# Kernel optimization log

Measured on AMD Instinct MI355X. Metric: run time of the kernel, lower is better.

Reference implementation:

```python
import jax, jax.numpy as jnp
import numpy as np

N0, N1, N2 = 100000, 25000, 6250
E0, E1, E2 = 600000, 150000, 40000
K = 6
NUM_CLASSES = 10


def setup_inputs() -> dict:
    key = jax.random.key(0)
    ks = jax.random.split(key, 20)
    inp = {
        "pos": jax.random.normal(ks[0], (N0, 3), dtype=jnp.float32),
        "edge_index0": jax.random.randint(ks[1], (2, E0), 0, N0, dtype=jnp.int32),
        "edge_index1": jax.random.randint(ks[2], (2, E1), 0, N1, dtype=jnp.int32),
        "edge_index2": jax.random.randint(ks[3], (2, E2), 0, N2, dtype=jnp.int32),
        "d0_rows": jax.random.randint(ks[4], (N0,), 0, N1, dtype=jnp.int32),
        "d0_cols": jax.random.randint(ks[5], (N0,), 0, N0, dtype=jnp.int32),
        "d0_vals": jax.random.uniform(ks[6], (N0,), dtype=jnp.float32),
        "d1_rows": jax.random.randint(ks[7], (N1,), 0, N2, dtype=jnp.int32),
        "d1_cols": jax.random.randint(ks[8], (N1,), 0, N1, dtype=jnp.int32),
        "d1_vals": jax.random.uniform(ks[9], (N1,), dtype=jnp.float32),
        "W0": jax.random.normal(ks[10], (K, 3, 32), dtype=jnp.float32) * 0.1,
        "b0": jax.random.normal(ks[11], (32,), dtype=jnp.float32) * 0.1,
        "W1": jax.random.normal(ks[12], (K, 32, 64), dtype=jnp.float32) * 0.1,
        "b1": jax.random.normal(ks[13], (64,), dtype=jnp.float32) * 0.1,
        "W2": jax.random.normal(ks[14], (K, 64, 128), dtype=jnp.float32) * 0.1,
        "b2": jax.random.normal(ks[15], (128,), dtype=jnp.float32) * 0.1,
        "lin_w": jax.random.normal(ks[16], (NUM_CLASSES, N2 * 128), dtype=jnp.float32) * 0.01,
        "lin_b": jax.random.normal(ks[17], (NUM_CLASSES,), dtype=jnp.float32) * 0.1,
    }
    return inp


def _cheb_edge_weights(row, col, n):
    # PyG get_laplacian(sym) followed by 2L/lambda_max - I with lambda_max=2:
    # diagonal becomes 0, off-diagonal weight = -deg^{-1/2}[row] * deg^{-1/2}[col]
    deg = jax.ops.segment_sum(jnp.ones(row.shape[0], jnp.float32), row, num_segments=n)
    dinv = jnp.where(deg > 0, 1.0 / jnp.sqrt(deg), 0.0)
    return -dinv[row] * dinv[col]


def _cheb_conv(x, edge_index, W, b, n):
    # Chebyshev recurrence: Tx0 = x, Tx1 = L_hat x, Tx_k = 2 L_hat Tx_{k-1} - Tx_{k-2}
    row, col = edge_index[0], edge_index[1]
    w = _cheb_edge_weights(row, col, n)

    def prop(z):  # [n, C] -> [n, C] scatter-gather over edges
        return jax.ops.segment_sum(w[:, None] * z[col], row, num_segments=n)

    Tx0 = x
    out = Tx0 @ W[0]
    Tx1 = prop(x)
    out = out + Tx1 @ W[1]
    for k in range(2, W.shape[0]):
        Tx2 = 2.0 * prop(Tx1) - Tx0
        out = out + Tx2 @ W[k]
        Tx0, Tx1 = Tx1, Tx2
    return out + b


def _pool(x, rows, cols, vals, n_out):
    # torch.sparse.mm(D, x) with D given in COO form
    return jax.ops.segment_sum(vals[:, None] * x[cols], rows, num_segments=n_out)


def reference(pos, edge_index0, edge_index1, edge_index2,
              d0_rows, d0_cols, d0_vals, d1_rows, d1_cols, d1_vals,
              W0, b0, W1, b1, W2, b2, lin_w, lin_b):
    x = jax.nn.relu(_cheb_conv(pos, edge_index0, W0, b0, N0))
    x = _pool(x, d0_rows, d0_cols, d0_vals, N1)
    x = jax.nn.relu(_cheb_conv(x, edge_index1, W1, b1, N1))
    x = _pool(x, d1_rows, d1_cols, d1_vals, N2)
    x = _cheb_conv(x, edge_index2, W2, b2, N2)  # no ReLU on last conv
    Z = lin_w @ x.reshape(-1) + lin_b
    return Z
```

## Files before the change

### kernel.cpp

```cpp
#include <hip/hip_runtime.h>


#define TPB 256
#define NB   318
#define BCAP 8192
#define EPB  4096
#define TXS  800000LL

static inline int gs(long long n) { return (int)((n + TPB - 1) / TPB); }

struct Desc5 {
    const int* rows[5];
    const int* cols[5];
    const float* vals[5];
    int eoff[6];
    int doff[5];
};


__global__ void k_binA_pad(Desc5 d, int* __restrict__ gbcnt, int2* __restrict__ binrec,
                           int Etot, int binBlocks,
                           const float* __restrict__ pos, float4* __restrict__ pdst,
                           int npos) {
    __shared__ int2 srec[EPB];
    __shared__ unsigned short sbuck[EPB];
    __shared__ int scnt[NB], sbase[NB], slcur[NB];
    int tid = threadIdx.x;
    if ((int)blockIdx.x >= binBlocks) {
        int i = (blockIdx.x - binBlocks) * 256 + tid;
        if (i < npos)
            pdst[i] = make_float4(pos[3 * i], pos[3 * i + 1], pos[3 * i + 2], 0.f);
        return;
    }
    int e0 = blockIdx.x * EPB;
    int ne = min(EPB, Etot - e0);
    for (int b = tid; b < NB; b += 256) scnt[b] = 0;
    __syncthreads();
    for (int i = tid; i < ne; i += 256) {
        int e = e0 + i;
        int s = 0;
        while (e >= d.eoff[s + 1]) ++s;
        int le = e - d.eoff[s];
        int grow = d.doff[s] + d.rows[s][le];
        int col = d.cols[s][le];
        int vb = (s >= 3) ? __float_as_int(d.vals[s][le]) : 0;
        int b = grow >> 9;
        srec[i] = make_int2(((grow & 511) << 17) | col, vb);
        sbuck[i] = (unsigned short)b;
        atomicAdd(&scnt[b], 1);
    }
    __syncthreads();
    for (int b = tid; b < NB; b += 256) {
        sbase[b] = scnt[b] > 0 ? atomicAdd(&gbcnt[b], scnt[b]) : 0;
        slcur[b] = 0;
    }
    __syncthreads();
    for (int i = tid; i < ne; i += 256) {
        int b = sbuck[i];
        int off = atomicAdd(&slcur[b], 1);
        binrec[(long long)b * BCAP + sbase[b] + off] = srec[i];
    }
}

__global__ void k_B1(const int* __restrict__ gbcnt, const int2* __restrict__ binrec,
                     int* __restrict__ rowptr, float* __restrict__ dinv,
                     int ntot, int ndinv, int Etot) {
    __shared__ int cnt[512], lexcl[512], wsum[4];
    int bucket = blockIdx.x, tid = threadIdx.x;
    int lane = tid & 63, wid = tid >> 6;
    {
        int v0 = (2 * tid < NB) ? gbcnt[2 * tid] : 0;
        int v1 = (2 * tid + 1 < NB) ? gbcnt[2 * tid + 1] : 0;
        int p = v0 + v1;
        int s = p;
#pragma unroll
        for (int off = 1; off < 64; off <<= 1) {
            int t = __shfl_up(s, off, 64);
            if (lane >= off) s += t;
        }
        if (lane == 63) wsum[wid] = s;
        __syncthreads();
        int add = 0;
        for (int w = 0; w < wid; ++w) add += wsum[w];
        int ep = add + s - p;
        lexcl[2 * tid] = ep; lexcl[2 * tid + 1] = ep + v0;
        __syncthreads();
    }
    int base = lexcl[bucket];
    __syncthreads();
    int ne = gbcnt[bucket];
    const int2* br = binrec + (long long)bucket * BCAP;
    cnt[2 * tid] = 0; cnt[2 * tid + 1] = 0;
    __syncthreads();
    for (int i = tid; i < ne; i += 256)
        atomicAdd(&cnt[br[i].x >> 17], 1);
    __syncthreads();
    int c0 = cnt[2 * tid], c1 = cnt[2 * tid + 1], p = c0 + c1;
    int s = p;
#pragma unroll
    for (int off = 1; off < 64; off <<= 1) {
        int t = __shfl_up(s, off, 64);
        if (lane >= off) s += t;
    }
    if (lane == 63) wsum[wid] = s;
    __syncthreads();
    int add = 0;
    for (int w = 0; w < wid; ++w) add += wsum[w];
    int ep = add + s - p;
    lexcl[2 * tid] = ep; lexcl[2 * tid + 1] = ep + c0;
    __syncthreads();
    int row0 = bucket << 9;
    int nrows = min(512, ntot - row0);
    for (int lr = tid; lr < nrows; lr += 256) {
        int grow = row0 + lr;
        rowptr[grow] = base + lexcl[lr];
        if (grow < ndinv) {
            int c = cnt[lr];
            dinv[grow] = c > 0 ? 1.0f / sqrtf((float)c) : 0.f;
        }
    }
    if (bucket == 0 && tid == 0) rowptr[ntot] = Etot;
}

__global__ void k_B2(const int* __restrict__ gbcnt, const int2* __restrict__ binrec,
                     const int* __restrict__ rowptr, const float* __restrict__ dinv,
                     int2* __restrict__ rec, int ntot) {
    __shared__ int lbase[512], lcur[512];
    int bucket = blockIdx.x, tid = threadIdx.x;
    int row0 = bucket << 9;
    for (int i = tid; i < 512; i += 256) {
        int grow = row0 + i;
        lbase[i] = (grow < ntot) ? rowptr[grow] : 0;
        lcur[i] = 0;
    }
    __syncthreads();
    int ne = gbcnt[bucket];
    const int2* br = binrec + (long long)bucket * BCAP;
    for (int i = tid; i < ne; i += 256) {
        int2 r = br[i];
        int lr = r.x >> 17, col = r.x & 0x1FFFF;
        int grow = row0 + lr;
        int pos = lbase[lr] + atomicAdd(&lcur[lr], 1);
        float wv;
        if (grow < 100000)      wv = dinv[col];
        else if (grow < 125000) wv = dinv[100000 + col];
        else if (grow < 131250) wv = dinv[125000 + col];
        else                    wv = __int_as_float(r.y);
        rec[pos] = make_int2(col, __float_as_int(wv));
    }
}


__global__ void k_sprop_c4p(const int* __restrict__ rowptr, const int2* __restrict__ rec,
                            const float* __restrict__ dinv, const float* __restrict__ src,
                            const float* __restrict__ prev, float* __restrict__ dst,
                            int n, int mode) {
    int idx = blockIdx.x * blockDim.x + threadIdx.x;
    if (idx >= 2 * n) return;
    int r = idx >> 1, half = idx & 1;
    int s0 = rowptr[r], s1 = rowptr[r + 1];
    float4 a0 = make_float4(0.f, 0.f, 0.f, 0.f), a1 = a0;
    int j = s0 + half;
    for (; j + 2 < s1; j += 4) {
        int2 r0 = rec[j], r1 = rec[j + 2];
        float w0 = __int_as_float(r0.y), w1 = __int_as_float(r1.y);
        float4 s0v = *(const float4*)(src + (long long)r0.x * 4);
        float4 s1v = *(const float4*)(src + (long long)r1.x * 4);
        a0.x += w0 * s0v.x; a0.y += w0 * s0v.y; a0.z += w0 * s0v.z; a0.w += w0 * s0v.w;
        a1.x += w1 * s1v.x; a1.y += w1 * s1v.y; a1.z += w1 * s1v.z; a1.w += w1 * s1v.w;
    }
    if (j < s1) {
        int2 rr = rec[j];
        float w = __int_as_float(rr.y);
        float4 s = *(const float4*)(src + (long long)rr.x * 4);
        a0.x += w * s.x; a0.y += w * s.y; a0.z += w * s.z; a0.w += w * s.w;
    }
    a0.x += a1.x; a0.y += a1.y; a0.z += a1.z; a0.w += a1.w;
    a0.x += __shfl_xor(a0.x, 1, 64);
    a0.y += __shfl_xor(a0.y, 1, 64);
    a0.z += __shfl_xor(a0.z, 1, 64);
    a0.w += __shfl_xor(a0.w, 1, 64);
    if (half == 0) {
        float m = -dinv[r];
        long long o = (long long)r * 4;
        float4 out;
        if (mode) {
            float4 p = *(const float4*)(prev + o);
            out.x = 2.f * m * a0.x - p.x; out.y = 2.f * m * a0.y - p.y;
            out.z = 2.f * m * a0.z - p.z; out.w = 2.f * m * a0.w - p.w;
        } else {
            out.x = m * a0.x; out.y = m * a0.y; out.z = m * a0.z; out.w = m * a0.w;
        }
        *(float4*)(dst + o) = out;
    }
}

__device__ __forceinline__
void sprop32p_body(const int* __restrict__ rowptr, const int2* __restrict__ rec,
                   const float* __restrict__ dinv, const float* __restrict__ src,
                   const float* __restrict__ prev, float* __restrict__ dst,
                   int n, int mode, int idx) {
    constexpr int C = 32;
    if (idx >= n * 8) return;
    int cid = idx >> 1, half = idx & 1;
    int r = cid >> 2, c4 = (cid & 3) * 8;
    int s0 = rowptr[r], s1 = rowptr[r + 1];
    float4 a0 = make_float4(0.f, 0.f, 0.f, 0.f), a1 = a0;
    for (int j = s0 + half; j < s1; j += 2) {
        int2 rr = rec[j];
        float w = __int_as_float(rr.y);
        const float* sp = src + (long long)rr.x * C + c4;
        float4 s0v = *(const float4*)(sp);
        float4 s1v = *(const float4*)(sp + 4);
        a0.x += w * s0v.x; a0.y += w * s0v.y; a0.z += w * s0v.z; a0.w += w * s0v.w;
        a1.x += w * s1v.x; a1.y += w * s1v.y; a1.z += w * s1v.z; a1.w += w * s1v.w;
    }
    a0.x += __shfl_xor(a0.x, 1, 64); a0.y += __shfl_xor(a0.y, 1, 64);
    a0.z += __shfl_xor(a0.z, 1, 64); a0.w += __shfl_xor(a0.w, 1, 64);
    a1.x += __shfl_xor(a1.x, 1, 64); a1.y += __shfl_xor(a1.y, 1, 64);
    a1.z += __shfl_xor(a1.z, 1, 64); a1.w += __shfl_xor(a1.w, 1, 64);
    if (half == 0) {
        float m = -dinv[r];
        long long o = (long long)r * C + c4;
        float4 o0, o1;
        if (mode) {
            float4 p0 = *(const float4*)(prev + o);
            float4 p1 = *(const float4*)(prev + o + 4);
            o0.x = 2.f * m * a0.x - p0.x; o0.y = 2.f * m * a0.y - p0.y;
            o0.z = 2.f * m * a0.z - p0.z; o0.w = 2.f * m * a0.w - p0.w;
            o1.x = 2.f * m * a1.x - p1.x; o1.y = 2.f * m * a1.y - p1.y;
            o1.z = 2.f * m * a1.z - p1.z; o1.w = 2.f * m * a1.w - p1.w;
        } else {
            o0.x = m * a0.x; o0.y = m * a0.y; o0.z = m * a0.z; o0.w = m * a0.w;
            o1.x = m * a1.x; o1.y = m * a1.y; o1.z = m * a1.z; o1.w = m * a1.w;
        }
        *(float4*)(dst + o) = o0;
        *(float4*)(dst + o + 4) = o1;
    }
}

__device__ __forceinline__
void sprop64p_body(const int* __restrict__ rowptr, const int2* __restrict__ rec,
                   const float* __restrict__ dinv, const float* __restrict__ src,
                   const float* __restrict__ prev, float* __restrict__ dst,
                   int n, int mode, int idx) {
    constexpr int C = 64, C4 = 16;
    if (idx >= n * C4 * 2) return;
    int cid = idx >> 1, half = idx & 1;
    int r = cid / C4, c4 = (cid - r * C4) * 4;
    int s0 = rowptr[r], s1 = rowptr[r + 1];
    float4 a0 = make_float4(0.f, 0.f, 0.f, 0.f), a1 = a0;
    int j = s0 + half;
    for (; j + 2 < s1; j += 4) {
        int2 r0 = rec[j], r1 = rec[j + 2];
        float w0 = __int_as_float(r0.y), w1 = __int_as_float(r1.y);
        float4 s0v = *(const float4*)(src + (long long)r0.x * C + c4);
        float4 s1v = *(const float4*)(src + (long long)r1.x * C + c4);
        a0.x += w0 * s0v.x; a0.y += w0 * s0v.y; a0.z += w0 * s0v.z; a0.w += w0 * s0v.w;
        a1.x += w1 * s1v.x; a1.y += w1 * s1v.y; a1.z += w1 * s1v.z; a1.w += w1 * s1v.w;
    }
    if (j < s1) {
        int2 rr = rec[j];
        float w = __int_as_float(rr.y);
        float4 s = *(const float4*)(src + (long long)rr.x * C + c4);
        a0.x += w * s.x; a0.y += w * s.y; a0.z += w * s.z; a0.w += w * s.w;
    }
    a0.x += a1.x; a0.y += a1.y; a0.z += a1.z; a0.w += a1.w;
    a0.x += __shfl_xor(a0.x, 1, 64); a0.y += __shfl_xor(a0.y, 1, 64);
    a0.z += __shfl_xor(a0.z, 1, 64); a0.w += __shfl_xor(a0.w, 1, 64);
    if (half == 0) {
        float m = -dinv[r];
        long long o = (long long)r * C + c4;
        float4 out;
        if (mode) {
            float4 p = *(const float4*)(prev + o);
            out.x = 2.f * m * a0.x - p.x; out.y = 2.f * m * a0.y - p.y;
            out.z = 2.f * m * a0.z - p.z; out.w = 2.f * m * a0.w - p.w;
        } else {
            out.x = m * a0.x; out.y = m * a0.y; out.z = m * a0.z; out.w = m * a0.w;
        }
        *(float4*)(dst + o) = out;
    }
}


template <int CIN, int COUT, int NT>
__device__ __forceinline__
void gemm1k_body(float* __restrict__ part, const float* __restrict__ txbase,
                 const float* __restrict__ W, int n, int pstride, int kg, int idx) {
    constexpr int CO4 = COUT / 4;
    int per = (n / NT) * CO4;
    if (idx >= per) return;
    int tile = idx / CO4, co = (idx - tile * CO4) * 4;
    int node0 = tile * NT;
    float4 acc[NT];
#pragma unroll
    for (int i = 0; i < NT; ++i) acc[i] = make_float4(0.f, 0.f, 0.f, 0.f);
    const float* xb = txbase + (long long)kg * TXS + (long long)node0 * CIN;
    const float* Wk = W + (long long)kg * CIN * COUT + co;
#pragma unroll 1
    for (int c4 = 0; c4 < CIN / 4; ++c4) {
        const float* Wr = Wk + c4 * 4 * COUT;
        float4 w0 = *(const float4*)(Wr);
        float4 w1 = *(const float4*)(Wr + COUT);
        float4 w2 = *(const float4*)(Wr + 2 * COUT);
        float4 w3 = *(const float4*)(Wr + 3 * COUT);
#pragma unroll
        for (int i = 0; i < NT; ++i) {
            float4 xv = *(const float4*)(xb + i * CIN + c4 * 4);
            acc[i].x += xv.x * w0.x + xv.y * w1.x + xv.z * w2.x + xv.w * w3.x;
            acc[i].y += xv.x * w0.y + xv.y * w1.y + xv.z * w2.y + xv.w * w3.y;
            acc[i].z += xv.x * w0.z + xv.y * w1.z + xv.z * w2.z + xv.w * w3.z;
            acc[i].w += xv.x * w0.w + xv.y * w1.w + xv.z * w2.w + xv.w * w3.w;
        }
    }
    float* op = part + (long long)kg * pstride + (long long)node0 * COUT + co;
#pragma unroll
    for (int i = 0; i < NT; ++i)
        *(float4*)(op + (long long)i * COUT) = acc[i];
}


__global__ __launch_bounds__(256, 4)
void k_pack1(const int* __restrict__ rowptr, const int2* __restrict__ rec,
             const float* __restrict__ dinv, const float* __restrict__ src,
             const float* __restrict__ prev, float* __restrict__ dst,
             int n, int mode, float* __restrict__ part,
             const float* __restrict__ txbase, const float* __restrict__ W,
             int pstride, int kg, int spropBlocks) {
    int bid = blockIdx.x;
    if (bid < spropBlocks)
        sprop32p_body(rowptr, rec, dinv, src, prev, dst, n, mode,
                      bid * 256 + threadIdx.x);
    else
        gemm1k_body<32, 64, 4>(part, txbase, W, n, pstride, kg,
                               (bid - spropBlocks) * 256 + threadIdx.x);
}

__global__ __launch_bounds__(256, 4)
void k_pack2(const int* __restrict__ rowptr, const int2* __restrict__ rec,
             const float* __restrict__ dinv, const float* __restrict__ src,
             const float* __restrict__ prev, float* __restrict__ dst,
             int n, int mode, float* __restrict__ part,
             const float* __restrict__ txbase, const float* __restrict__ W,
             int pstride, int kg, int spropBlocks) {
    int bid = blockIdx.x;
    if (bid < spropBlocks)
        sprop64p_body(rowptr, rec, dinv, src, prev, dst, n, mode,
                      bid * 256 + threadIdx.x);
    else
        gemm1k_body<64, 128, 2>(part, txbase, W, n, pstride, kg,
                                (bid - spropBlocks) * 256 + threadIdx.x);
}

template <int CIN, int COUT, int NT>
__global__ __launch_bounds__(256, 4)
void k_gemm1k(float* __restrict__ part, const float* __restrict__ txbase,
              const float* __restrict__ W, int n, int pstride, int kg) {
    gemm1k_body<CIN, COUT, NT>(part, txbase, W, n, pstride, kg,
                               blockIdx.x * 256 + threadIdx.x);
}

__global__ __launch_bounds__(256, 4)
void k_conv0_final(const int* __restrict__ rowptr, const int2* __restrict__ rec,
                   const float* __restrict__ dinv, const float* __restrict__ txbase,
                   const float* __restrict__ W, const float* __restrict__ b,
                   float* __restrict__ out, int n) {
    int r = blockIdx.x * blockDim.x + threadIdx.x;
    if (r >= n) return;
    const float* src = txbase + 4 * TXS;
    int s0 = rowptr[r], s1 = rowptr[r + 1];
    float4 a0 = make_float4(0.f, 0.f, 0.f, 0.f);
    float4 a1 = a0;
    int j = s0;
    if ((j & 1) && j < s1) {
        int2 rr = rec[j];
        float w = __int_as_float(rr.y);
        float4 s = *(const float4*)(src + (long long)rr.x * 4);
        a0.x += w * s.x; a0.y += w * s.y; a0.z += w * s.z;
        ++j;
    }
    for (; j + 2 <= s1; j += 2) {
        int4 q = *(const int4*)(rec + j);
        float wa = __int_as_float(q.y), wb = __int_as_float(q.w);
        float4 sa = *(const float4*)(src + (long long)q.x * 4);
        float4 sb = *(const float4*)(src + (long long)q.z * 4);
        a0.x += wa * sa.x; a0.y += wa * sa.y; a0.z += wa * sa.z;
        a1.x += wb * sb.x; a1.y += wb * sb.y; a1.z += wb * sb.z;
    }
    if (j < s1) {
        int2 rr = rec[j];
        float w = __int_as_float(rr.y);
        float4 s = *(const float4*)(src + (long long)rr.x * 4);
        a0.x += w * s.x; a0.y += w * s.y; a0.z += w * s.z;
    }
    a0.x += a1.x; a0.y += a1.y; a0.z += a1.z;
    float m = -dinv[r];
    float4 xv[6];
#pragma unroll
    for (int k = 0; k < 5; ++k)
        xv[k] = *(const float4*)(txbase + (long long)k * TXS + (long long)r * 4);
    xv[5].x = 2.f * m * a0.x - xv[3].x;
    xv[5].y = 2.f * m * a0.y - xv[3].y;
    xv[5].z = 2.f * m * a0.z - xv[3].z;
    float* op = out + (long long)r * 32;
#pragma unroll 1
    for (int co4 = 0; co4 < 8; ++co4) {
        float4 acc = *(const float4*)(b + co4 * 4);
#pragma unroll
        for (int k = 0; k < 6; ++k) {
            const float* Wk = W + k * 96 + co4 * 4;
            float4 w0 = *(const float4*)(Wk);
            float4 w1 = *(const float4*)(Wk + 32);
            float4 w2 = *(const float4*)(Wk + 64);
            acc.x += xv[k].x * w0.x + xv[k].y * w1.x + xv[k].z * w2.x;
            acc.y += xv[k].x * w0.y + xv[k].y * w1.y + xv[k].z * w2.y;
            acc.z += xv[k].x * w0.z + xv[k].y * w1.z + xv[k].z * w2.z;
            acc.w += xv[k].x * w0.w + xv[k].y * w1.w + xv[k].z * w2.w;
        }
        *(float4*)(op + co4 * 4) = acc;
    }
}


template <int C>
__global__ void k_spool4_t(const int* __restrict__ rowptr, const int2* __restrict__ rec,
                           const float* __restrict__ x, float* __restrict__ out, int n) {
    constexpr int C4 = C / 4;
    int idx = blockIdx.x * blockDim.x + threadIdx.x;
    if (idx >= n * C4) return;
    int r = idx / C4, c4 = (idx - r * C4) * 4;
    int s0 = rowptr[r], s1 = rowptr[r + 1];
    float4 acca = make_float4(0.f, 0.f, 0.f, 0.f);
    float4 accb = make_float4(0.f, 0.f, 0.f, 0.f);
    int j = s0;
    if ((j & 1) && j < s1) {
        int2 rr = rec[j];
        float v = __int_as_float(rr.y);
        float4 s = *(const float4*)(x + (long long)rr.x * C + c4);
        acca.x += v * fmaxf(s.x, 0.f); acca.y += v * fmaxf(s.y, 0.f);
        acca.z += v * fmaxf(s.z, 0.f); acca.w += v * fmaxf(s.w, 0.f);
        ++j;
    }
    for (; j + 2 <= s1; j += 2) {
        int4 q = *(const int4*)(rec + j);
        float va = __int_as_float(q.y), vb = __int_as_float(q.w);
        float4 sa = *(const float4*)(x + (long long)q.x * C + c4);
        float4 sb = *(const float4*)(x + (long long)q.z * C + c4);
        acca.x += va * fmaxf(sa.x, 0.f); acca.y += va * fmaxf(sa.y, 0.f);
        acca.z += va * fmaxf(sa.z, 0.f); acca.w += va * fmaxf(sa.w, 0.f);
        accb.x += vb * fmaxf(sb.x, 0.f); accb.y += vb * fmaxf(sb.y, 0.f);
        accb.z += vb * fmaxf(sb.z, 0.f); accb.w += vb * fmaxf(sb.w, 0.f);
    }
    if (j < s1) {
        int2 rr = rec[j];
        float v = __int_as_float(rr.y);
        float4 s = *(const float4*)(x + (long long)rr.x * C + c4);
        acca.x += v * fmaxf(s.x, 0.f); acca.y += v * fmaxf(s.y, 0.f);
        acca.z += v * fmaxf(s.z, 0.f); acca.w += v * fmaxf(s.w, 0.f);
    }
    acca.x += accb.x; acca.y += accb.y; acca.z += accb.z; acca.w += accb.w;
    *(float4*)(out + (long long)r * C + c4) = acca;
}


template <int C, int KSPLIT>
__global__ void k_pool_f(const int* __restrict__ rowptr, const int2* __restrict__ rec,
                         const float* __restrict__ part, const float* __restrict__ bias,
                         float* __restrict__ out, int n, int partStride) {
    constexpr int C4 = C / 4;
    int idx = blockIdx.x * blockDim.x + threadIdx.x;
    if (idx >= n * C4) return;
    int r = idx / C4, c4 = (idx - r * C4) * 4;
    int s0 = rowptr[r], s1 = rowptr[r + 1];
    float4 bb = *(const float4*)(bias + c4);
    float4 acc = make_float4(0.f, 0.f, 0.f, 0.f);
    for (int j = s0; j < s1; ++j) {
        int2 rr = rec[j];
        float v = __int_as_float(rr.y);
        float4 x = bb;
#pragma unroll
        for (int s = 0; s < KSPLIT; ++s) {
            float4 p = *(const float4*)(part + (long long)s * partStride + (long long)rr.x * C + c4);
            x.x += p.x; x.y += p.y; x.z += p.z; x.w += p.w;
        }
        acc.x += v * fmaxf(x.x, 0.f); acc.y += v * fmaxf(x.y, 0.f);
        acc.z += v * fmaxf(x.z, 0.f); acc.w += v * fmaxf(x.w, 0.f);
    }
    *(float4*)(out + (long long)r * C + c4) = acc;
}


__global__ void k_linear_partial_f(const float* __restrict__ lw,
                                   const float4* __restrict__ part,
                                   const float* __restrict__ b2,
                                   float* __restrict__ partials,
                                   int len4, int len, int nblk) {
    float acc[10];
#pragma unroll
    for (int j = 0; j < 10; ++j) acc[j] = 0.f;
    const float4* b2v = (const float4*)b2;
    for (int i = blockIdx.x * blockDim.x + threadIdx.x; i < len4;
         i += gridDim.x * blockDim.x) {
        float4 xv = b2v[i & 31];
#pragma unroll
        for (int s = 0; s < 6; ++s) {
            float4 p = part[s * 200000 + i];
            xv.x += p.x; xv.y += p.y; xv.z += p.z; xv.w += p.w;
        }
#pragma unroll
        for (int j = 0; j < 10; ++j) {
            float4 wv = *(const float4*)(lw + (long long)j * len + i * 4);
            acc[j] += xv.x * wv.x + xv.y * wv.y + xv.z * wv.z + xv.w * wv.w;
        }
    }
    __shared__ float lds[4][10];
    int wid = threadIdx.x >> 6, lane = threadIdx.x & 63;
#pragma unroll
    for (int j = 0; j < 10; ++j) {
        float v = acc[j];
        for (int off = 32; off > 0; off >>= 1) v += __shfl_down(v, off, 64);
        if (lane == 0) lds[wid][j] = v;
    }
    __syncthreads();
    if (threadIdx.x < 10) {
        float s = lds[0][threadIdx.x] + lds[1][threadIdx.x] +
                  lds[2][threadIdx.x] + lds[3][threadIdx.x];
        partials[threadIdx.x * nblk + blockIdx.x] = s;
    }
}

__global__ void k_linear_final(const float* __restrict__ partials,
                               const float* __restrict__ lb,
                               float* __restrict__ out, int nblk) {
    int j = threadIdx.x >> 6, lane = threadIdx.x & 63;
    float v = 0.f;
    for (int b = lane; b < nblk; b += 64) v += partials[j * nblk + b];
    for (int off = 32; off > 0; off >>= 1) v += __shfl_down(v, off, 64);
    if (lane == 0) out[j] = lb[j] + v;
}

extern "C" void kernel_launch(void* const* d_in, const int* in_sizes, int n_in,
                              void* d_out, int out_size, void* d_ws, size_t ws_size,
                              hipStream_t stream) {
    const int cN0 = 100000, cN1 = 25000, cN2 = 6250;
    const int cE0 = 600000, cE1 = 150000, cE2 = 40000;
    const int NBLK = 512;

    const float* pos = (const float*)d_in[0];
    const int*   ei0 = (const int*)d_in[1];
    const int*   ei1 = (const int*)d_in[2];
    const int*   ei2 = (const int*)d_in[3];
    const int*   d0r = (const int*)d_in[4];
    const int*   d0c = (const int*)d_in[5];
    const float* d0v = (const float*)d_in[6];
    const int*   d1r = (const int*)d_in[7];
    const int*   d1c = (const int*)d_in[8];
    const float* d1v = (const float*)d_in[9];
    const float* W0  = (const float*)d_in[10];
    const float* b0  = (const float*)d_in[11];
    const float* W1  = (const float*)d_in[12];
    const float* b1  = (const float*)d_in[13];
    const float* W2  = (const float*)d_in[14];
    const float* b2  = (const float*)d_in[15];
    const float* lw  = (const float*)d_in[16];
    const float* lb  = (const float*)d_in[17];
    float* outZ = (float*)d_out;

    const int ntot = cN0 + cN1 + cN2 + cN1 + cN2;
    const int Etot = cE0 + cE1 + cE2 + cN0 + cN1;
    const int Eg   = cE0 + cE1 + cE2;
    const int ndinv = cN0 + cN1 + cN2;
    const int doff0 = 0, doff1 = cN0, doff2 = cN0 + cN1,
              doffp0 = doff2 + cN2, doffp1 = doffp0 + cN1;

    int*   iws    = (int*)d_ws;
    int*   gbcnt  = iws;
    int*   rowptr = gbcnt + 320;
    float* dinv   = (float*)(rowptr + 162504);
    int2*  binrec = (int2*)(dinv + 131256);
    int2*  rec    = binrec + (long long)NB * BCAP;
    float* txbuf  = (float*)(rec + 915000);
    float* part   = txbuf + 6 * TXS;
    float* bufOut = part + 9600000;
    float* lpart  = bufOut + 3200000;

    Desc5 d;
    d.rows[0] = ei0;        d.cols[0] = ei0 + cE0; d.vals[0] = nullptr;
    d.rows[1] = ei1;        d.cols[1] = ei1 + cE1; d.vals[1] = nullptr;
    d.rows[2] = ei2;        d.cols[2] = ei2 + cE2; d.vals[2] = nullptr;
    d.rows[3] = d0r;        d.cols[3] = d0c;       d.vals[3] = d0v;
    d.rows[4] = d1r;        d.cols[4] = d1c;       d.vals[4] = d1v;
    d.eoff[0] = 0;
    d.eoff[1] = cE0;
    d.eoff[2] = cE0 + cE1;
    d.eoff[3] = Eg;
    d.eoff[4] = Eg + cN0;
    d.eoff[5] = Etot;
    d.doff[0] = doff0; d.doff[1] = doff1; d.doff[2] = doff2;
    d.doff[3] = doffp0; d.doff[4] = doffp1;

    hipMemsetAsync(gbcnt, 0, (size_t)NB * 4, stream);
    int binBlocks = (Etot + EPB - 1) / EPB;
    int padBlocks = gs(cN0);
    k_binA_pad<<<binBlocks + padBlocks, TPB, 0, stream>>>(
        d, gbcnt, binrec, Etot, binBlocks, pos, (float4*)txbuf, cN0);
    k_B1<<<NB, TPB, 0, stream>>>(gbcnt, binrec, rowptr, dinv, ntot, ndinv, Etot);
    k_B2<<<NB, TPB, 0, stream>>>(gbcnt, binrec, rowptr, dinv, rec, ntot);

    for (int k = 1; k <= 4; ++k) {
        const float* src = txbuf + (long long)(k - 1) * TXS;
        const float* prev = (k >= 2) ? txbuf + (long long)(k - 2) * TXS : nullptr;
        float* dst = txbuf + (long long)k * TXS;
        k_sprop_c4p<<<gs((long long)cN0 * 2), TPB, 0, stream>>>(
            rowptr + doff0, rec, dinv + doff0, src, prev, dst, cN0, k >= 2 ? 1 : 0);
    }
    k_conv0_final<<<gs(cN0), TPB, 0, stream>>>(
        rowptr + doff0, rec, dinv + doff0, txbuf, W0, b0, bufOut, cN0);
    k_spool4_t<32><<<gs((long long)cN1 * 8), TPB, 0, stream>>>(
        rowptr + doffp0, rec, bufOut, txbuf, cN1);

    {
        const int pstride = cN1 * 64;
        int sB = gs((long long)cN1 * 8);
        int gB = gs((long long)(cN1 / 4) * 16);
        for (int k = 1; k <= 5; ++k) {
            const float* src = txbuf + (long long)(k - 1) * TXS;
            const float* prev = (k >= 2) ? txbuf + (long long)(k - 2) * TXS : nullptr;
            float* dst = txbuf + (long long)k * TXS;
            k_pack1<<<sB + gB, TPB, 0, stream>>>(
                rowptr + doff1, rec, dinv + doff1, src, prev, dst, cN1,
                k >= 2 ? 1 : 0, part, txbuf, W1, pstride, k - 1, sB);
        }
        k_gemm1k<32, 64, 4><<<gB, TPB, 0, stream>>>(part, txbuf, W1, cN1, pstride, 5);
        k_pool_f<64, 6><<<gs((long long)cN2 * 16), TPB, 0, stream>>>(
            rowptr + doffp1, rec, part, b1, txbuf, cN2, pstride);
    }

    {
        const int pstride = cN2 * 128;
        int sB = gs((long long)cN2 * 32);
        int gB = gs((long long)(cN2 / 2) * 32);
        for (int k = 1; k <= 5; ++k) {
            const float* src = txbuf + (long long)(k - 1) * TXS;
            const float* prev = (k >= 2) ? txbuf + (long long)(k - 2) * TXS : nullptr;
            float* dst = txbuf + (long long)k * TXS;
            k_pack2<<<sB + gB, TPB, 0, stream>>>(
                rowptr + doff2, rec, dinv + doff2, src, prev, dst, cN2,
                k >= 2 ? 1 : 0, part, txbuf, W2, pstride, k - 1, sB);
        }
        k_gemm1k<64, 128, 2><<<gB, TPB, 0, stream>>>(part, txbuf, W2, cN2, pstride, 5);
        k_linear_partial_f<<<NBLK, TPB, 0, stream>>>(
            lw, (const float4*)part, b2, lpart, cN2 * 128 / 4, cN2 * 128, NBLK);
        k_linear_final<<<1, 640, 0, stream>>>(lpart, lb, outZ, NBLK);
    }
}
```

Measured before the change: 254.3 us.

## Fuse last Chebyshev propagation with its weight GEMM in conv1 and conv2

For conv1 and conv2, the final Chebyshev step (k=5) is no longer written to the Tx buffer and then multiplied by a separate GEMM kernel. A new fused kernel computes Tx5 per row tile into shared memory and immediately multiplies it by W[5] into the partial output. The same launch also carries the k=4 GEMM blocks. This removes one launch per layer and the round trip of Tx5 through global memory, at the cost of extra shared memory and a redundant per-block W read.

```diff
diff --git a/kernel.cpp b/kernel.cpp
--- a/kernel.cpp
+++ b/kernel.cpp
@@ -353,12 +353,165 @@
                                 (bid - spropBlocks) * 256 + threadIdx.x);
 }
 
-template <int CIN, int COUT, int NT>
+
+__device__ __forceinline__
+void convf1_body(const int* __restrict__ rowptr, const int2* __restrict__ rec,
+                 const float* __restrict__ dinv, const float* __restrict__ txbase,
+                 const float* __restrict__ W, float* __restrict__ part,
+                 int n, int pstride, int bid, float (*ltx)[36]) {
+    constexpr int C = 32;
+    int tid = threadIdx.x;
+    int row0 = bid * 32;
+    const float* src = txbase + 4 * TXS;
+    const float* prv = txbase + 3 * TXS;
+    {
+        int rl = tid >> 3, c4 = (tid & 7) * 4;
+        int r = row0 + rl;
+        if (r < n) {
+            int s0 = rowptr[r], s1 = rowptr[r + 1];
+            float4 a0 = make_float4(0.f, 0.f, 0.f, 0.f), a1 = a0;
+            int j = s0;
+            for (; j + 2 <= s1; j += 2) {
+                int2 q0 = rec[j], q1 = rec[j + 1];
+                float w0 = __int_as_float(q0.y), w1 = __int_as_float(q1.y);
+                float4 s0v = *(const float4*)(src + (long long)q0.x * C + c4);
+                float4 s1v = *(const float4*)(src + (long long)q1.x * C + c4);
+                a0.x += w0 * s0v.x; a0.y += w0 * s0v.y; a0.z += w0 * s0v.z; a0.w += w0 * s0v.w;
+                a1.x += w1 * s1v.x; a1.y += w1 * s1v.y; a1.z += w1 * s1v.z; a1.w += w1 * s1v.w;
+            }
+            if (j < s1) {
+                int2 q = rec[j];
+                float w = __int_as_float(q.y);
+                float4 s = *(const float4*)(src + (long long)q.x * C + c4);
+                a0.x += w * s.x; a0.y += w * s.y; a0.z += w * s.z; a0.w += w * s.w;
+            }
+            a0.x += a1.x; a0.y += a1.y; a0.z += a1.z; a0.w += a1.w;
+            float m = -dinv[r];
+            float4 p = *(const float4*)(prv + (long long)r * C + c4);
+            ltx[rl][c4]     = 2.f * m * a0.x - p.x;
+            ltx[rl][c4 + 1] = 2.f * m * a0.y - p.y;
+            ltx[rl][c4 + 2] = 2.f * m * a0.z - p.z;
+            ltx[rl][c4 + 3] = 2.f * m * a0.w - p.w;
+        }
+    }
+    __syncthreads();
+    const float* Wk = W + 5 * 32 * 64;
+#pragma unroll
+    for (int half = 0; half < 2; ++half) {
+        int out_id = half * 256 + tid;
+        int rl = out_id >> 4, co = (out_id & 15) * 4;
+        int r = row0 + rl;
+        if (r >= n) continue;
+        float4 acc = make_float4(0.f, 0.f, 0.f, 0.f);
+#pragma unroll 1
+        for (int c4 = 0; c4 < 8; ++c4) {
+            const float* Wr = Wk + c4 * 4 * 64 + co;
+            float4 w0 = *(const float4*)(Wr);
+            float4 w1 = *(const float4*)(Wr + 64);
+            float4 w2 = *(const float4*)(Wr + 128);
+            float4 w3 = *(const float4*)(Wr + 192);
+            float4 xv = *(const float4*)(&ltx[rl][c4 * 4]);
+            acc.x += xv.x * w0.x + xv.y * w1.x + xv.z * w2.x + xv.w * w3.x;
+            acc.y += xv.x * w0.y + xv.y * w1.y + xv.z * w2.y + xv.w * w3.y;
+            acc.z += xv.x * w0.z + xv.y * w1.z + xv.z * w2.z + xv.w * w3.z;
+            acc.w += xv.x * w0.w + xv.y * w1.w + xv.z * w2.w + xv.w * w3.w;
+        }
+        *(float4*)(part + 5LL * pstride + (long long)r * 64 + co) = acc;
+    }
+}
+
+__device__ __forceinline__
+void convf2_body(const int* __restrict__ rowptr, const int2* __restrict__ rec,
+                 const float* __restrict__ dinv, const float* __restrict__ txbase,
+                 const float* __restrict__ W, float* __restrict__ part,
+                 int n, int pstride, int bid, float (*ltx)[68]) {
+    constexpr int C = 64;
+    int tid = threadIdx.x;
+    int row0 = bid * 16;
+    const float* src = txbase + 4 * TXS;
+    const float* prv = txbase + 3 * TXS;
+    {
+        int rl = tid >> 4, c4 = (tid & 15) * 4;
+        int r = row0 + rl;
+        if (r < n) {
+            int s0 = rowptr[r], s1 = rowptr[r + 1];
+            float4 a0 = make_float4(0.f, 0.f, 0.f, 0.f), a1 = a0;
+            int j = s0;
+            for (; j + 2 <= s1; j += 2) {
+                int2 q0 = rec[j], q1 = rec[j + 1];
+                float w0 = __int_as_float(q0.y), w1 = __int_as_float(q1.y);
+                float4 s0v = *(const float4*)(src + (long long)q0.x * C + c4);
+                float4 s1v = *(const float4*)(src + (long long)q1.x * C + c4);
+                a0.x += w0 * s0v.x; a0.y += w0 * s0v.y; a0.z += w0 * s0v.z; a0.w += w0 * s0v.w;
+                a1.x += w1 * s1v.x; a1.y += w1 * s1v.y; a1.z += w1 * s1v.z; a1.w += w1 * s1v.w;
+            }
+            if (j < s1) {
+                int2 q = rec[j];
+                float w = __int_as_float(q.y);
+                float4 s = *(const float4*)(src + (long long)q.x * C + c4);
+                a0.x += w * s.x; a0.y += w * s.y; a0.z += w * s.z; a0.w += w * s.w;
+            }
+            a0.x += a1.x; a0.y += a1.y; a0.z += a1.z; a0.w += a1.w;
+            float m = -dinv[r];
+            float4 p = *(const float4*)(prv + (long long)r * C + c4);
+            ltx[rl][c4]     = 2.f * m * a0.x - p.x;
+            ltx[rl][c4 + 1] = 2.f * m * a0.y - p.y;
+            ltx[rl][c4 + 2] = 2.f * m * a0.z - p.z;
+            ltx[rl][c4 + 3] = 2.f * m * a0.w - p.w;
+        }
+    }
+    __syncthreads();
+    const float* Wk = W + 5 * 64 * 128;
+#pragma unroll
+    for (int half = 0; half < 2; ++half) {
+        int out_id = half * 256 + tid;
+        int rl = out_id >> 5, co = (out_id & 31) * 4;
+        int r = row0 + rl;
+        if (r >= n) continue;
+        float4 acc = make_float4(0.f, 0.f, 0.f, 0.f);
+#pragma unroll 1
+        for (int c4 = 0; c4 < 16; ++c4) {
+            const float* Wr = Wk + c4 * 4 * 128 + co;
+            float4 w0 = *(const float4*)(Wr);
+            float4 w1 = *(const float4*)(Wr + 128);
+            float4 w2 = *(const float4*)(Wr + 256);
+            float4 w3 = *(const float4*)(Wr + 384);
+            float4 xv = *(const float4*)(&ltx[rl][c4 * 4]);
+            acc.x += xv.x * w0.x + xv.y * w1.x + xv.z * w2.x + xv.w * w3.x;
+            acc.y += xv.x * w0.y + xv.y * w1.y + xv.z * w2.y + xv.w * w3.y;
+            acc.z += xv.x * w0.z + xv.y * w1.z + xv.z * w2.z + xv.w * w3.z;
+            acc.w += xv.x * w0.w + xv.y * w1.w + xv.z * w2.w + xv.w * w3.w;
+        }
+        *(float4*)(part + 5LL * pstride + (long long)r * 128 + co) = acc;
+    }
+}
+
 __global__ __launch_bounds__(256, 4)
-void k_gemm1k(float* __restrict__ part, const float* __restrict__ txbase,
-              const float* __restrict__ W, int n, int pstride, int kg) {
-    gemm1k_body<CIN, COUT, NT>(part, txbase, W, n, pstride, kg,
-                               blockIdx.x * 256 + threadIdx.x);
+void k_packf1(const int* __restrict__ rowptr, const int2* __restrict__ rec,
+              const float* __restrict__ dinv, const float* __restrict__ txbase,
+              const float* __restrict__ W, float* __restrict__ part,
+              int n, int pstride, int fB) {
+    __shared__ float ltx[32][36];
+    int bid = blockIdx.x;
+    if (bid < fB)
+        convf1_body(rowptr, rec, dinv, txbase, W, part, n, pstride, bid, ltx);
+    else
+        gemm1k_body<32, 64, 4>(part, txbase, W, n, pstride, 4,
+                               (bid - fB) * 256 + threadIdx.x);
+}
+
+__global__ __launch_bounds__(256, 4)
+void k_packf2(const int* __restrict__ rowptr, const int2* __restrict__ rec,
+              const float* __restrict__ dinv, const float* __restrict__ txbase,
+              const float* __restrict__ W, float* __restrict__ part,
+              int n, int pstride, int fB) {
+    __shared__ float ltx[16][68];
+    int bid = blockIdx.x;
+    if (bid < fB)
+        convf2_body(rowptr, rec, dinv, txbase, W, part, n, pstride, bid, ltx);
+    else
+        gemm1k_body<64, 128, 2>(part, txbase, W, n, pstride, 4,
+                                (bid - fB) * 256 + threadIdx.x);
 }
 
 __global__ __launch_bounds__(256, 4)
@@ -624,7 +777,7 @@
         const int pstride = cN1 * 64;
         int sB = gs((long long)cN1 * 8);
         int gB = gs((long long)(cN1 / 4) * 16);
-        for (int k = 1; k <= 5; ++k) {
+        for (int k = 1; k <= 4; ++k) {
             const float* src = txbuf + (long long)(k - 1) * TXS;
             const float* prev = (k >= 2) ? txbuf + (long long)(k - 2) * TXS : nullptr;
             float* dst = txbuf + (long long)k * TXS;
@@ -632,7 +785,9 @@
                 rowptr + doff1, rec, dinv + doff1, src, prev, dst, cN1,
                 k >= 2 ? 1 : 0, part, txbuf, W1, pstride, k - 1, sB);
         }
-        k_gemm1k<32, 64, 4><<<gB, TPB, 0, stream>>>(part, txbuf, W1, cN1, pstride, 5);
+        int fB = (cN1 + 31) / 32;
+        k_packf1<<<fB + gB, TPB, 0, stream>>>(
+            rowptr + doff1, rec, dinv + doff1, txbuf, W1, part, cN1, pstride, fB);
         k_pool_f<64, 6><<<gs((long long)cN2 * 16), TPB, 0, stream>>>(
             rowptr + doffp1, rec, part, b1, txbuf, cN2, pstride);
     }
@@ -641,7 +796,7 @@
         const int pstride = cN2 * 128;
         int sB = gs((long long)cN2 * 32);
         int gB = gs((long long)(cN2 / 2) * 32);
-        for (int k = 1; k <= 5; ++k) {
+        for (int k = 1; k <= 4; ++k) {
             const float* src = txbuf + (long long)(k - 1) * TXS;
             const float* prev = (k >= 2) ? txbuf + (long long)(k - 2) * TXS : nullptr;
             float* dst = txbuf + (long long)k * TXS;
@@ -649,7 +804,9 @@
                 rowptr + doff2, rec, dinv + doff2, src, prev, dst, cN2,
                 k >= 2 ? 1 : 0, part, txbuf, W2, pstride, k - 1, sB);
         }
-        k_gemm1k<64, 128, 2><<<gB, TPB, 0, stream>>>(part, txbuf, W2, cN2, pstride, 5);
+        int fB = (cN2 + 15) / 16;
+        k_packf2<<<fB + gB, TPB, 0, stream>>>(
+            rowptr + doff2, rec, dinv + doff2, txbuf, W2, part, cN2, pstride, fB);
         k_linear_partial_f<<<NBLK, TPB, 0, stream>>>(
             lw, (const float4*)part, b2, lpart, cN2 * 128 / 4, cN2 * 128, NBLK);
         k_linear_final<<<1, 640, 0, stream>>>(lpart, lb, outZ, NBLK);
```

New measurement: 253.0 us. No clear change (-0.5%).
